# Performance work log

Measured on AMD Instinct MI355X. Metric: run time of the kernel, lower is better.

## Reference

```python
import jax, jax.numpy as jnp
import numpy as np

B, T, X, H, Z, Y, G = 4096, 32, 256, 256, 128, 2, 128


def setup_inputs() -> dict:
    key = jax.random.key(0)
    ks = jax.random.split(key, 16)
    rn = lambda k, s, sc=0.05: jax.random.normal(k, s, dtype=jnp.float32) * sc
    n_days = jnp.concatenate([jnp.array([T], dtype=jnp.int32),
                              jax.random.randint(ks[2], (B - 1,), 1, T + 1).astype(jnp.int32)])
    return {
        "x": rn(ks[0], (B, T, X), 1.0),
        "y_true": jax.nn.softmax(jax.random.normal(ks[1], (B, T, Y), dtype=jnp.float32), axis=-1),
        "n_days": n_days,
        "z0": rn(ks[3], (B, Z), 1.0),
        "eps": rn(ks[4], (T, B, Z), 1.0),
        "W_ih": rn(ks[5], (3 * H, X)), "W_hh": rn(ks[6], (3 * H, H)),
        "b_ih": jnp.zeros((3 * H,), jnp.float32), "b_hh": jnp.zeros((3 * H,), jnp.float32),
        "Wph": rn(ks[7], (Z, X + H + Z)), "bph": jnp.zeros((Z,), jnp.float32),
        "Woh": rn(ks[8], (Z, X + H + Y + Z)), "boh": jnp.zeros((Z,), jnp.float32),
        "Wpm": rn(ks[9], (Z, Z)), "bpm": jnp.zeros((Z,), jnp.float32),
        "Wps": rn(ks[10], (Z, Z)), "bps": jnp.zeros((Z,), jnp.float32),
        "Wqm": rn(ks[11], (Z, Z)), "bqm": jnp.zeros((Z,), jnp.float32),
        "Wqs": rn(ks[12], (Z, Z)), "bqs": jnp.zeros((Z,), jnp.float32),
        "Wg": rn(ks[13], (G, H + Z)), "bg": jnp.zeros((G,), jnp.float32),
        "Wy": rn(ks[14], (Y, G)), "by": jnp.zeros((Y,), jnp.float32),
    }


def _forward(x, y_true, z0, eps, W_ih, W_hh, b_ih, b_hh, Wph, bph, Woh, boh,
             Wpm, bpm, Wps, bps, Wqm, bqm, Wqs, bqs, Wg, bg, Wy, by, n_days):
    xt = jnp.transpose(x, (1, 0, 2))       # [T, B, X]
    yt = jnp.transpose(y_true, (1, 0, 2))  # [T, B, Y]

    # --- GRU over time (torch nn.GRU gate math) ---
    def gru_step(h, xi):
        gi = xi @ W_ih.T + b_ih
        gh = h @ W_hh.T + b_hh
        ir, iz, inn = jnp.split(gi, 3, axis=-1)
        hr, hz, hn = jnp.split(gh, 3, axis=-1)
        r = jax.nn.sigmoid(ir + hr)
        u = jax.nn.sigmoid(iz + hz)
        n = jnp.tanh(inn + r * hn)
        h_new = (1.0 - u) * n + u * h
        return h_new, h_new

    h0 = jnp.zeros((x.shape[0], H), x.dtype)
    _, hs = jax.lax.scan(gru_step, h0, xt)  # [T, B, H]
    # pack/pad semantics: padded timesteps produce zero outputs
    valid = jnp.arange(T)[:, None] < n_days[None, :]  # [T, B]
    hs = jnp.where(valid[:, :, None], hs, 0.0)

    # --- sequential VAE latent scan: z_t depends on z_{t-1} ---
    def vmd_step(z, inputs):
        xi, hi, yi, ei = inputs
        hzp = jnp.tanh(jnp.concatenate([xi, hi, z], -1) @ Wph.T + bph)
        mp = hzp @ Wpm.T + bpm
        sp = jnp.sqrt(jnp.exp(hzp @ Wps.T + bps))
        hzq = jnp.tanh(jnp.concatenate([xi, hi, yi, z], -1) @ Woh.T + boh)
        mq = hzq @ Wqm.T + bqm
        sq = jnp.sqrt(jnp.exp(hzq @ Wqs.T + bqs))
        z_post = mq + sq * ei
        # kl_normal_normal(post || prior)
        kl = jnp.log(sp / sq) + (sq * sq + (mq - mp) ** 2) / (2.0 * sp * sp) - 0.5
        return z_post, (z_post, kl)

    _, (z_posts, kls_e) = jax.lax.scan(vmd_step, z0, (xt, hs, yt, eps))
    kls = jnp.sum(kls_e, axis=-1).T  # [B, T]

    hz = jnp.concatenate([jnp.transpose(hs, (1, 0, 2)),
                          jnp.transpose(z_posts, (1, 0, 2))], -1)  # [B, T, H+Z]
    g = jnp.tanh(hz @ Wg.T + bg)                     # [B, T, G]
    y_pred = jax.nn.softmax(g @ Wy.T + by, axis=-1)  # [B, T, Y]

    idx = n_days - 1
    b = jnp.arange(x.shape[0])
    g_T = g[b, idx]       # [B, G]
    y_T = y_pred[b, idx]  # [B, Y]
    return jnp.concatenate([g_T, y_T, kls], axis=-1)  # [B, G+Y+T]


def reference(x, y_true, n_days, z0, eps, W_ih, W_hh, b_ih, b_hh, Wph, bph,
              Woh, boh, Wpm, bpm, Wps, bps, Wqm, bqm, Wqs, bqs, Wg, bg, Wy, by):
    return _forward(x, y_true, z0, eps, W_ih, W_hh, b_ih, b_hh, Wph, bph, Woh,
                    boh, Wpm, bpm, Wps, bps, Wqm, bqm, Wqs, bqs, Wg, bg, Wy, by,
                    n_days)
```

## Files before the change

### kernel.cpp

```cpp
#include <hip/hip_runtime.h>

typedef unsigned short u16;
typedef short bf16x8 __attribute__((ext_vector_type(8)));
typedef float f32x4 __attribute__((ext_vector_type(4)));

__device__ __forceinline__ float bf2f(u16 v){
  union { unsigned u; float f; } x; x.u = ((unsigned)v) << 16; return x.f;
}
__device__ __forceinline__ u16 f2bf(float f){
  union { float f; unsigned u; } x; x.f = f;
  unsigned u = x.u;
  u += 0x7fffu + ((u >> 16) & 1u);
  return (u16)(u >> 16);
}
__device__ __forceinline__ unsigned pk_bf16(float lo, float hi){
  unsigned r;
  asm volatile("v_cvt_pk_bf16_f32 %0, %1, %2" : "=v"(r) : "v"(lo), "v"(hi));
  return r;
}
__device__ __forceinline__ float sigm(float x){ return 1.f/(1.f+__expf(-x)); }
__device__ __forceinline__ float tanh_s(float x){ return 1.f - 2.f/(__expf(2.f*x)+1.f); }
__device__ __forceinline__ f32x4 mfma16(bf16x8 a, bf16x8 b, f32x4 c){
  return __builtin_amdgcn_mfma_f32_16x16x32_bf16(a, b, c, 0, 0, 0);
}
__device__ __forceinline__ void gl2lds16(const void* g, void* l){
  __builtin_amdgcn_global_load_lds(
      (const __attribute__((address_space(1))) unsigned int*)g,
      (__attribute__((address_space(3))) unsigned int*)l, 16, 0, 0);
}

__global__ void prep_w(const float* __restrict__ W_ih, const float* __restrict__ W_hh,
                       const float* __restrict__ Wph, const float* __restrict__ Woh,
                       const float* __restrict__ Wpm, const float* __restrict__ Wps,
                       const float* __restrict__ Wqm, const float* __restrict__ Wqs,
                       const float* __restrict__ Wg,  const float* __restrict__ bph,
                       const float* __restrict__ boh,
                       u16* __restrict__ wsb, float* __restrict__ Woy, float* __restrict__ bpq)
{
  int idx = blockIdx.x*256 + threadIdx.x;
  if (idx < 196608){ wsb[idx] = f2bf(W_ih[idx]); return; }
  if (idx < 393216){ wsb[idx] = f2bf(W_hh[idx-196608]); return; }
  if (idx < 524288){ int j = idx-393216; int row = j>>9, col = j&511;
    float v = (row<128) ? Wph[row*640+col] : Woh[(row-128)*642+col];
    wsb[idx] = f2bf(v); return; }
  if (idx < 540672){ int j = idx-524288; int row=j>>7, col=j&127; wsb[idx]=f2bf(Wph[row*640+512+col]); return; }
  if (idx < 557056){ int j = idx-540672; int row=j>>7, col=j&127; wsb[idx]=f2bf(Woh[row*642+514+col]); return; }
  if (idx < 573440){ wsb[idx]=f2bf(Wpm[idx-557056]); return; }
  if (idx < 589824){ wsb[idx]=f2bf(Wps[idx-573440]); return; }
  if (idx < 606208){ wsb[idx]=f2bf(Wqm[idx-589824]); return; }
  if (idx < 622592){ wsb[idx]=f2bf(Wqs[idx-606208]); return; }
  if (idx < 671744){ wsb[idx]=f2bf(Wg[idx-622592]); return; }
  if (idx < 672000){ int j = idx-671744; int row=j>>1; Woy[j] = Woh[row*642+512+(j&1)]; return; }
  if (idx < 672256){ int j = idx-672000; bpq[j] = (j<128) ? bph[j] : boh[j-128]; return; }
}

__global__ void prep_b(const float* __restrict__ b_ih, const float* __restrict__ b_hh,
                       float* __restrict__ bsum)
{
  int j = threadIdx.x;
  if (j < 768) bsum[j] = b_ih[j] + (j < 512 ? b_hh[j] : 0.f);
}

__global__ void prep_x(const float* __restrict__ x, u16* __restrict__ xbf){
  int i = blockIdx.x*256 + threadIdx.x;
  if (i >= 4194304) return;
  const float4* src = (const float4*)(x + (size_t)i*8);
  float4 a = src[0], b = src[1];
  uint4 o;
  o.x = pk_bf16(a.x, a.y);
  o.y = pk_bf16(a.z, a.w);
  o.z = pk_bf16(b.x, b.y);
  o.w = pk_bf16(b.z, b.w);
  ((uint4*)xbf)[i] = o;
}

__global__ void sort_days(const int* __restrict__ n_days, int* __restrict__ perm,
                          int* __restrict__ nd_s, int* __restrict__ cnt)
{
  __shared__ int hist[34];
  __shared__ int base[34];
  __shared__ int cursor[34];
  int tid = threadIdx.x;
  if (tid < 34) hist[tid] = 0;
  __syncthreads();
  for (int i = tid; i < 4096; i += 1024) atomicAdd(&hist[n_days[i]], 1);
  __syncthreads();
  if (tid == 0){
    int acc = 0;
    for (int v = 32; v >= 1; --v){ base[v] = acc; acc += hist[v]; }
    base[0] = acc;
  }
  __syncthreads();
  if (tid < 33) cursor[tid] = base[tid];
  if (tid < 32) cnt[tid] = base[tid];
  __syncthreads();
  for (int i = tid; i < 4096; i += 1024){
    int v = n_days[i];
    int pos = atomicAdd(&cursor[v], 1);
    perm[pos] = i;
    nd_s[pos] = v;
  }
}

__global__ __launch_bounds__(512, 4) void gemm_gi(
  const u16* __restrict__ A, const u16* __restrict__ W,
  const float* __restrict__ bias, const int* __restrict__ perm,
  const int* __restrict__ cnt, u16* __restrict__ C)
{
  const int t  = blockIdx.x >> 5;
  const int rt = blockIdx.x & 31;
  if (rt*128 >= cnt[t]) return;
  const int n0 = blockIdx.y*256;
  const int tid = threadIdx.x;
  const int w = tid>>6, lane = tid&63, c = lane&15, g = lane>>4;
  const int wm = w>>2, wn = w&3;
  __shared__ __align__(16) char smem[49152];
  u16* abuf = (u16*)smem;
  u16* wbuf = (u16*)(smem + 16384);
  u16* clds = (u16*)smem;

  size_t asrc[2];
  #pragma unroll
  for (int i=0;i<2;++i){
    int p = (w*2+i)*64 + lane;
    int k8 = p>>7, row = p&127;
    asrc[i] = ((size_t)perm[rt*128 + row]*32 + t)*256 + k8*8;
  }
  size_t wsrc[4];
  #pragma unroll
  for (int i=0;i<4;++i){
    int p = (w*4+i)*64 + lane;
    int k8 = p>>8, row = p&255;
    wsrc[i] = (size_t)(n0+row)*256 + k8*8;
  }
  f32x4 acc[4][4];
  #pragma unroll
  for (int i=0;i<4;++i)
    #pragma unroll
    for (int j=0;j<4;++j) acc[i][j] = (f32x4){0.f,0.f,0.f,0.f};
  for (int kc=0; kc<4; ++kc){
    __syncthreads();
    #pragma unroll
    for (int i=0;i<2;++i) gl2lds16(A + asrc[i] + kc*64, &abuf[(w*2+i)*512]);
    #pragma unroll
    for (int i=0;i<4;++i) gl2lds16(W + wsrc[i] + kc*64, &wbuf[(w*4+i)*512]);
    __syncthreads();
    #pragma unroll
    for (int ks=0;ks<2;++ks){
      int k8 = ks*4 + g;
      bf16x8 a[4];
      #pragma unroll
      for (int mt=0;mt<4;++mt) a[mt] = *(const bf16x8*)&abuf[(k8*128 + wm*64 + mt*16 + c)*8];
      #pragma unroll
      for (int nt=0;nt<4;++nt){
        bf16x8 b = *(const bf16x8*)&wbuf[(k8*256 + wn*64 + nt*16 + c)*8];
        #pragma unroll
        for (int mt=0;mt<4;++mt)
          acc[mt][nt] = mfma16(a[mt], b, acc[mt][nt]);
      }
    }
  }
  __syncthreads();
  const size_t crow = (size_t)t*4096 + rt*128;
  #pragma unroll
  for (int nh=0; nh<2; ++nh){
    if ((wn>>1) == nh){
      #pragma unroll
      for (int nt=0;nt<4;++nt){
        int n = n0 + wn*64 + nt*16 + c;
        float bn = bias[n];
        int lc = (wn&1)*64 + nt*16 + c;
        #pragma unroll
        for (int mt=0;mt<4;++mt){
          int lr = wm*64 + mt*16 + g*4;
          #pragma unroll
          for (int r=0;r<4;++r)
            clds[(lr+r)*136 + lc] = f2bf(acc[mt][nt][r] + bn);
        }
      }
    }
    __syncthreads();
    #pragma unroll
    for (int p=0;p<4;++p){
      int idx = p*512 + tid;
      int row = idx>>4, ch = idx&15;
      *(uint4*)(C + (crow+row)*768 + n0 + nh*128 + ch*8)
        = *(const uint4*)&clds[row*136 + ch*8];
    }
    __syncthreads();
  }
}

__global__ __launch_bounds__(512, 4) void gemm_hpq(
  const u16* __restrict__ A1, const u16* __restrict__ A2,
  const u16* __restrict__ W, const float* __restrict__ bias,
  const float* __restrict__ yt, const float* __restrict__ Woy,
  u16* __restrict__ C)
{
  const int m0 = blockIdx.x*128;
  const int tid = threadIdx.x;
  const int w = tid>>6, lane = tid&63, c = lane&15, g = lane>>4;
  const int wm = w>>2, wn = w&3;
  __shared__ __align__(16) char smem[49152];
  u16* abuf = (u16*)smem;
  u16* wbuf = (u16*)(smem + 16384);
  u16* clds = (u16*)smem;

  size_t asrc[2];
  #pragma unroll
  for (int i=0;i<2;++i){
    int p = (w*2+i)*64 + lane;
    int k8 = p>>7, row = p&127;
    asrc[i] = (size_t)(m0+row)*256 + k8*8;
  }
  size_t wsrc[4];
  #pragma unroll
  for (int i=0;i<4;++i){
    int p = (w*4+i)*64 + lane;
    int k8 = p>>8, row = p&255;
    wsrc[i] = (size_t)row*512 + k8*8;
  }
  f32x4 acc[4][4];
  #pragma unroll
  for (int i=0;i<4;++i)
    #pragma unroll
    for (int j=0;j<4;++j) acc[i][j] = (f32x4){0.f,0.f,0.f,0.f};
  for (int kc=0; kc<8; ++kc){
    __syncthreads();
    const u16* Ab = (kc < 4) ? A1 : A2;
    int ko = (kc & 3)*64;
    #pragma unroll
    for (int i=0;i<2;++i) gl2lds16(Ab + asrc[i] + ko, &abuf[(w*2+i)*512]);
    #pragma unroll
    for (int i=0;i<4;++i) gl2lds16(W + wsrc[i] + kc*64, &wbuf[(w*4+i)*512]);
    __syncthreads();
    #pragma unroll
    for (int ks=0;ks<2;++ks){
      int k8 = ks*4 + g;
      bf16x8 a[4];
      #pragma unroll
      for (int mt=0;mt<4;++mt) a[mt] = *(const bf16x8*)&abuf[(k8*128 + wm*64 + mt*16 + c)*8];
      #pragma unroll
      for (int nt=0;nt<4;++nt){
        bf16x8 b = *(const bf16x8*)&wbuf[(k8*256 + wn*64 + nt*16 + c)*8];
        #pragma unroll
        for (int mt=0;mt<4;++mt)
          acc[mt][nt] = mfma16(a[mt], b, acc[mt][nt]);
      }
    }
  }
  __syncthreads();
  #pragma unroll
  for (int nh=0; nh<2; ++nh){
    if ((wn>>1) == nh){
      #pragma unroll
      for (int nt=0;nt<4;++nt){
        int n = wn*64 + nt*16 + c;
        float bn = bias[n];
        float wy0 = 0.f, wy1 = 0.f;
        bool yfl = (n >= 128);
        if (yfl){ wy0 = Woy[(n-128)*2]; wy1 = Woy[(n-128)*2+1]; }
        int lc = (wn&1)*64 + nt*16 + c;
        #pragma unroll
        for (int mt=0;mt<4;++mt){
          int lr = wm*64 + mt*16 + g*4;
          #pragma unroll
          for (int r=0;r<4;++r){
            size_t m = (size_t)m0 + lr + r;
            float v = acc[mt][nt][r] + bn;
            if (yfl) v += yt[2*m]*wy0 + yt[2*m+1]*wy1;
            clds[(lr+r)*136 + lc] = f2bf(v);
          }
        }
      }
    }
    __syncthreads();
    #pragma unroll
    for (int p=0;p<4;++p){
      int idx = p*512 + tid;
      int row = idx>>4, ch = idx&15;
      *(uint4*)(C + (size_t)(m0+row)*256 + nh*128 + ch*8)
        = *(const uint4*)&clds[row*136 + ch*8];
    }
    __syncthreads();
  }
}

__global__ __launch_bounds__(1024, 4) void gru_seq(
  const u16* __restrict__ GI, const u16* __restrict__ Whh,
  const float* __restrict__ bhh, const int* __restrict__ perm,
  const int* __restrict__ nd_s, u16* __restrict__ hs)
{
  const int b0 = blockIdx.x*16;
  const int tid = threadIdx.x;
  const int w = tid>>6, lane = tid&63, c = lane&15, g = lane>>4;
  const int j0 = w*16 + g*4;
  __shared__ __align__(16) u16 hbuf[2][4096];
  __shared__ __align__(16) u16 gibuf[3][12288];
  __shared__ float bhnl[256];

  bf16x8 wa[3][8];
  #pragma unroll
  for (int gate=0; gate<3; ++gate)
    #pragma unroll
    for (int ks=0; ks<8; ++ks)
      wa[gate][ks] = *(const bf16x8*)&Whh[(size_t)(gate*256 + w*16 + c)*256 + ks*32 + g*8];

  if (tid < 256) bhnl[tid] = bhh[512 + tid];
  const int ndc   = nd_s[b0 + c];
  const int bound = nd_s[b0];
  const int ob    = perm[b0 + c];

  int so0, so1;
  { int pe = w*512 + lane*8; int row = pe/768, off = pe - row*768;
    so0 = (b0+row)*768 + (off ^ ((row&7)<<3)); }
  { int pe = (16+w)*512 + lane*8; int row = pe/768, off = pe - row*768;
    so1 = (b0+row)*768 + (off ^ ((row&7)<<3)); }
  const int rd0 = c*1536 + ((j0*2) ^ ((c&7)<<4));
  const int hroff = (g*16 + c)*16;
  const int hwoff = ((w*2 + (g>>1))*16 + c)*16 + (g&1)*8;
  u16* hsp = hs + (size_t)ob*8192 + j0;

  float hprev[4] = {0.f,0.f,0.f,0.f};
  if (tid < 512) ((uint4*)hbuf[0])[tid] = make_uint4(0,0,0,0);

  const size_t PL = 3145728;
  int p1 = (bound > 1) ? 1 : 0;
  gl2lds16(GI + so0, (char*)gibuf[0] + w*1024);
  if (w < 8) gl2lds16(GI + so1, (char*)gibuf[0] + (16+w)*1024);
  gl2lds16(GI + (size_t)p1*PL + so0, (char*)gibuf[1] + w*1024);
  if (w < 8) gl2lds16(GI + (size_t)p1*PL + so1, (char*)gibuf[1] + (16+w)*1024);
  asm volatile("s_waitcnt vmcnt(0)" ::: "memory");
  __syncthreads();

  const u16* hr = hbuf[0];
  u16*       hw = hbuf[1];
  int cur = 0;
  #pragma unroll 1
  for (int t=0; t<bound; ++t){
    {
      int pf = (t+2 < bound) ? t+2 : bound-1;
      int nxt3 = cur >= 1 ? cur-1 : 2;
      gl2lds16(GI + (size_t)pf*PL + so0, (char*)gibuf[nxt3] + w*1024);
      if (w < 8) gl2lds16(GI + (size_t)pf*PL + so1, (char*)gibuf[nxt3] + (16+w)*1024);
    }
    const char* gib = (const char*)gibuf[cur];
    ushort4 gr_ = *(const ushort4*)(gib + rd0);
    ushort4 gu_ = *(const ushort4*)(gib + rd0 + 512);
    ushort4 gn_ = *(const ushort4*)(gib + rd0 + 1024);
    if (w < 8) asm volatile("s_waitcnt vmcnt(3)" ::: "memory");
    else       asm volatile("s_waitcnt vmcnt(2)" ::: "memory");
    __builtin_amdgcn_sched_barrier(0);
    f32x4 aR = (f32x4){0.f,0.f,0.f,0.f};
    f32x4 aU = (f32x4){0.f,0.f,0.f,0.f};
    float4 bhn4 = *(const float4*)&bhnl[j0];
    f32x4 aN = (f32x4){bhn4.x, bhn4.y, bhn4.z, bhn4.w};
    __builtin_amdgcn_s_setprio(1);
    #pragma unroll
    for (int ks=0; ks<8; ++ks){
      bf16x8 hf = *(const bf16x8*)((const char*)hr + hroff + ks*1024);
      aR = mfma16(wa[0][ks], hf, aR);
      aU = mfma16(wa[1][ks], hf, aU);
      aN = mfma16(wa[2][ks], hf, aN);
    }
    __builtin_amdgcn_s_setprio(0);
    {
      float h4[4];
      #pragma unroll
      for (int r=0; r<4; ++r){
        u16 grv = r==0?gr_.x : r==1?gr_.y : r==2?gr_.z : gr_.w;
        u16 guv = r==0?gu_.x : r==1?gu_.y : r==2?gu_.z : gu_.w;
        u16 gnv = r==0?gn_.x : r==1?gn_.y : r==2?gn_.z : gn_.w;
        float rr = sigm(bf2f(grv) + aR[r]);
        float uu = sigm(bf2f(guv) + aU[r]);
        float nn = tanh_s(bf2f(gnv) + rr*aN[r]);
        float h = nn + uu*(hprev[r]-nn);
        hprev[r] = h;
        h4[r] = h;
      }
      uint2 hpk;
      hpk.x = pk_bf16(h4[0], h4[1]);
      hpk.y = pk_bf16(h4[2], h4[3]);
      *(uint2*)((char*)hw + hwoff) = hpk;
      uint2 hst = (t < ndc) ? hpk : make_uint2(0u,0u);
      *(uint2*)(hsp + t*256) = hst;
    }
    asm volatile("s_waitcnt lgkmcnt(0)" ::: "memory");
    __builtin_amdgcn_sched_barrier(0);
    __builtin_amdgcn_s_barrier();
    __builtin_amdgcn_sched_barrier(0);
    { const u16* tmp = hr; hr = hw; hw = (u16*)tmp; }
    cur = cur==2 ? 0 : cur+1;
  }
  for (int t=bound; t<32; ++t)
    *(uint2*)(hsp + t*256) = make_uint2(0u,0u);
}

__global__ __launch_bounds__(512) void vae_seq(
  const u16* __restrict__ HPQ, const float* __restrict__ z0,
  const float* __restrict__ eps, const int* __restrict__ n_days,
  const u16* __restrict__ Wm,
  const float* __restrict__ bpm, const float* __restrict__ bps,
  const float* __restrict__ bqm, const float* __restrict__ bqs,
  u16* __restrict__ zidx, float* __restrict__ out)
{
  const int b0 = blockIdx.x*16;
  const int tid = threadIdx.x, w = tid>>6, lane = tid&63, c = lane&15, g = lane>>4;
  const int j0 = w*16 + g*4;
  __shared__ __align__(16) u16 zbuf[16*16*8];
  __shared__ __align__(16) u16 hzpb[16*16*8];
  __shared__ __align__(16) u16 hzqb[16*16*8];
  __shared__ __align__(16) char hpql[3][8192];
  __shared__ __align__(16) char epsl[3][8192];
  __shared__ float klb[32][16][8];

  bf16x8 wf[6][4];
  #pragma unroll
  for (int mat=0;mat<6;++mat)
    #pragma unroll
    for (int ks=0;ks<4;++ks)
      wf[mat][ks] = *(const bf16x8*)&Wm[mat*16384 + (w*16+c)*128 + ks*32 + g*8];

  const float4 bpm4 = *(const float4*)(bpm + j0);
  const float4 bps4 = *(const float4*)(bps + j0);
  const float4 bqm4 = *(const float4*)(bqm + j0);
  const float4 bqs4 = *(const float4*)(bqs + j0);
  const int ndc = n_days[b0 + c];

  int soH, soE;
  { int p = (w*64 + lane)*16; int row = p/512, off = p%512;
    int so = off ^ ((row&7)<<4);
    soH = (b0+row)*32*256 + (so>>1);
    soE = (b0+row)*128 + (so>>2); }
  const int rdH = c*512 + ((j0*2) ^ ((c&7)<<4));
  const int rdE = c*512 + ((j0*4) ^ ((c&7)<<4));
  const int hroff = (g*16 + c)*16;
  const int hwoff = ((w*2 + (g>>1))*16 + c)*16 + (g&1)*8;

  if (tid < 256){
    int k8 = tid>>4, row = tid&15;
    const float* zp = z0 + (size_t)(b0+row)*128 + k8*8;
    uint4 o;
    o.x = pk_bf16(zp[0], zp[1]);
    o.y = pk_bf16(zp[2], zp[3]);
    o.z = pk_bf16(zp[4], zp[5]);
    o.w = pk_bf16(zp[6], zp[7]);
    ((uint4*)zbuf)[tid] = o;
  }
  gl2lds16(HPQ + soH,          hpql[0] + w*1024);
  gl2lds16(eps + soE,          epsl[0] + w*1024);
  gl2lds16(HPQ + soH + 256,    hpql[1] + w*1024);
  gl2lds16(eps + soE + 524288, epsl[1] + w*1024);
  asm volatile("s_waitcnt vmcnt(0)" ::: "memory");
  __syncthreads();

  uint2 zsel = make_uint2(0u,0u);
  int cur = 0;
  #pragma unroll 1
  for (int t=0; t<32; ++t){
    if (t < 30){
      int nxt3 = cur >= 1 ? cur-1 : 2;
      gl2lds16(HPQ + soH + (t+2)*256,            hpql[nxt3] + w*1024);
      gl2lds16(eps + soE + (size_t)(t+2)*524288, epsl[nxt3] + w*1024);
    }
    if (t < 30)      { asm volatile("s_waitcnt vmcnt(2)" ::: "memory"); }
    else if (t == 30){ asm volatile("s_waitcnt vmcnt(0)" ::: "memory"); }
    __builtin_amdgcn_sched_barrier(0);
    f32x4 accP = (f32x4){0,0,0,0}, accQ = (f32x4){0,0,0,0};
    #pragma unroll
    for (int ks=0;ks<4;++ks){
      bf16x8 zf = *(const bf16x8*)((const char*)zbuf + hroff + ks*1024);
      accP = mfma16(wf[0][ks], zf, accP);
      accQ = mfma16(wf[1][ks], zf, accQ);
    }
    {
      const char* hb_ = hpql[cur];
      ushort4 hp4 = *(const ushort4*)(hb_ + rdH);
      ushort4 hq4 = *(const ushort4*)(hb_ + rdH + 256);
      float p4[4], q4[4];
      #pragma unroll
      for (int r=0;r<4;++r){
        u16 pv = r==0?hp4.x : r==1?hp4.y : r==2?hp4.z : hp4.w;
        u16 qv = r==0?hq4.x : r==1?hq4.y : r==2?hq4.z : hq4.w;
        p4[r] = tanh_s(bf2f(pv) + accP[r]);
        q4[r] = tanh_s(bf2f(qv) + accQ[r]);
      }
      uint2 ppk, qpk;
      ppk.x = pk_bf16(p4[0], p4[1]);  ppk.y = pk_bf16(p4[2], p4[3]);
      qpk.x = pk_bf16(q4[0], q4[1]);  qpk.y = pk_bf16(q4[2], q4[3]);
      *(uint2*)((char*)hzpb + hwoff) = ppk;
      *(uint2*)((char*)hzqb + hwoff) = qpk;
    }
    asm volatile("s_waitcnt lgkmcnt(0)" ::: "memory");
    __builtin_amdgcn_sched_barrier(0);
    __builtin_amdgcn_s_barrier();
    __builtin_amdgcn_sched_barrier(0);
    {
      f32x4 aMP=(f32x4){0,0,0,0}, aAP=(f32x4){0,0,0,0};
      f32x4 aMQ=(f32x4){0,0,0,0}, aAQ=(f32x4){0,0,0,0};
      #pragma unroll
      for (int ks=0;ks<4;++ks){
        bf16x8 pf = *(const bf16x8*)((const char*)hzpb + hroff + ks*1024);
        bf16x8 qf = *(const bf16x8*)((const char*)hzqb + hroff + ks*1024);
        aMP = mfma16(wf[2][ks], pf, aMP);
        aAP = mfma16(wf[3][ks], pf, aAP);
        aMQ = mfma16(wf[4][ks], qf, aMQ);
        aAQ = mfma16(wf[5][ks], qf, aAQ);
      }
      float4 e4 = *(const float4*)(epsl[cur] + rdE);
      float kls = 0.f;
      float z4[4];
      #pragma unroll
      for (int r=0;r<4;++r){
        float mp = aMP[r]+(r==0?bpm4.x:r==1?bpm4.y:r==2?bpm4.z:bpm4.w);
        float ap = aAP[r]+(r==0?bps4.x:r==1?bps4.y:r==2?bps4.z:bps4.w);
        float mq = aMQ[r]+(r==0?bqm4.x:r==1?bqm4.y:r==2?bqm4.z:bqm4.w);
        float aq = aAQ[r]+(r==0?bqs4.x:r==1?bqs4.y:r==2?bqs4.z:bqs4.w);
        float ev = r==0?e4.x : r==1?e4.y : r==2?e4.z : e4.w;
        float z = mq + __expf(0.5f*aq)*ev;
        float d = mq - mp;
        kls += 0.5f*(ap-aq) + 0.5f*(__expf(aq)+d*d)*__expf(-ap) - 0.5f;
        z4[r] = z;
      }
      uint2 zpk;
      zpk.x = pk_bf16(z4[0], z4[1]);
      zpk.y = pk_bf16(z4[2], z4[3]);
      *(uint2*)((char*)zbuf + hwoff) = zpk;
      if (t == ndc-1) zsel = zpk;
      kls += __shfl_xor(kls, 16);
      kls += __shfl_xor(kls, 32);
      if (lane < 16) klb[t][c][w] = kls;
    }
    asm volatile("s_waitcnt lgkmcnt(0)" ::: "memory");
    __builtin_amdgcn_sched_barrier(0);
    __builtin_amdgcn_s_barrier();
    __builtin_amdgcn_sched_barrier(0);
    cur = cur==2 ? 0 : cur+1;
  }
  *(uint2*)(zidx + (size_t)(b0+c)*128 + j0) = zsel;
  {
    int t2 = tid>>4, c2 = tid&15;
    float s = 0.f;
    #pragma unroll
    for (int ww=0;ww<8;++ww) s += klb[t2][c2][ww];
    out[(size_t)(b0+c2)*162 + 130 + t2] = s;
  }
}

__global__ __launch_bounds__(128) void head_k(
  const u16* __restrict__ hs, const u16* __restrict__ zidx,
  const int* __restrict__ n_days, const u16* __restrict__ Wgb,
  const float* __restrict__ bg, const float* __restrict__ Wy,
  const float* __restrict__ by, float* __restrict__ out)
{
  const int b = blockIdx.x;
  const int tid = threadIdx.x;
  const int lane = tid & 63, wv = tid >> 6;
  __shared__ float hz[384];
  __shared__ float red[2][2];
  const int idx = n_days[b]-1;
  const u16* hrow = hs + ((size_t)b*32 + idx)*256;
  for (int k=tid; k<256; k+=128) hz[k] = bf2f(hrow[k]);
  hz[256+tid] = bf2f(zidx[(size_t)b*128 + tid]);
  __syncthreads();
  const u16* wrow = Wgb + (size_t)tid*384;
  float s = 0.f;
  #pragma unroll 4
  for (int k8=0;k8<48;++k8){
    bf16x8 wvv = *(const bf16x8*)&wrow[k8*8];
    #pragma unroll
    for (int e=0;e<8;++e) s += bf2f((u16)wvv[e]) * hz[k8*8+e];
  }
  float gv = tanh_s(s + bg[tid]);
  out[(size_t)b*162 + tid] = gv;
  float a0 = gv*Wy[tid], a1 = gv*Wy[128+tid];
  #pragma unroll
  for (int off=1; off<64; off<<=1){
    a0 += __shfl_xor(a0, off);
    a1 += __shfl_xor(a1, off);
  }
  if (lane == 0){ red[0][wv] = a0; red[1][wv] = a1; }
  __syncthreads();
  if (tid == 0){
    float l0 = by[0] + red[0][0] + red[0][1];
    float l1 = by[1] + red[1][0] + red[1][1];
    float mx = fmaxf(l0,l1);
    float e0 = __expf(l0-mx), e1 = __expf(l1-mx);
    float si = e0+e1;
    out[(size_t)b*162 + 128] = e0/si;
    out[(size_t)b*162 + 129] = e1/si;
  }
}

extern "C" void kernel_launch(void* const* d_in, const int* in_sizes, int n_in,
                              void* d_out, int out_size, void* d_ws, size_t ws_size,
                              hipStream_t stream)
{
  const float* x      = (const float*)d_in[0];
  const float* y_true = (const float*)d_in[1];
  const int*   n_days = (const int*)d_in[2];
  const float* z0     = (const float*)d_in[3];
  const float* eps    = (const float*)d_in[4];
  const float* W_ih   = (const float*)d_in[5];
  const float* W_hh   = (const float*)d_in[6];
  const float* b_ih   = (const float*)d_in[7];
  const float* b_hh   = (const float*)d_in[8];
  const float* Wph    = (const float*)d_in[9];
  const float* bph    = (const float*)d_in[10];
  const float* Woh    = (const float*)d_in[11];
  const float* boh    = (const float*)d_in[12];
  const float* Wpm    = (const float*)d_in[13];
  const float* bpm    = (const float*)d_in[14];
  const float* Wps    = (const float*)d_in[15];
  const float* bps    = (const float*)d_in[16];
  const float* Wqm    = (const float*)d_in[17];
  const float* bqm    = (const float*)d_in[18];
  const float* Wqs    = (const float*)d_in[19];
  const float* bqs    = (const float*)d_in[20];
  const float* Wg     = (const float*)d_in[21];
  const float* bg     = (const float*)d_in[22];
  const float* Wy     = (const float*)d_in[23];
  const float* by     = (const float*)d_in[24];
  (void)in_sizes; (void)n_in; (void)out_size; (void)ws_size;

  u16*   wsb = (u16*)d_ws;
  float* wsf = (float*)d_ws;
  int*   wsi = (int*)d_ws;
  u16* Wih_b = wsb + 0;
  u16* Whh_b = wsb + 196608;
  u16* Wc_b  = wsb + 393216;
  u16* Wz_b  = wsb + 524288;
  u16* Wg_b  = wsb + 622592;
  float* Woy  = wsf + 335872;
  float* bpq  = wsf + 336128;
  float* bsum = wsf + 336384;
  int* perm   = wsi + 337152;
  int* nd_s   = wsi + 341248;
  int* cnt    = wsi + 345344;
  u16* xbf   = wsb + 690752;
  u16* GI    = wsb + 34245184;
  u16* hsB   = wsb + 134908480;
  u16* HPQ   = wsb + 168462912;
  u16* zidx  = wsb + 202017344;

  hipLaunchKernelGGL(prep_w, dim3(2626), dim3(256), 0, stream,
                     W_ih, W_hh, Wph, Woh, Wpm, Wps, Wqm, Wqs, Wg, bph, boh,
                     wsb, Woy, bpq);
  hipLaunchKernelGGL(prep_b, dim3(1), dim3(768), 0, stream, b_ih, b_hh, bsum);
  hipLaunchKernelGGL(prep_x, dim3(16384), dim3(256), 0, stream, x, xbf);
  hipLaunchKernelGGL(sort_days, dim3(1), dim3(1024), 0, stream,
                     n_days, perm, nd_s, cnt);
  hipLaunchKernelGGL(gemm_gi, dim3(1024,3), dim3(512), 0, stream,
                     xbf, Wih_b, bsum, perm, cnt, GI);
  hipLaunchKernelGGL(gru_seq, dim3(256), dim3(1024), 0, stream,
                     GI, Whh_b, b_hh, perm, nd_s, hsB);
  hipLaunchKernelGGL(gemm_hpq, dim3(1024), dim3(512), 0, stream,
                     xbf, hsB, Wc_b, bpq, y_true, Woy, HPQ);
  hipLaunchKernelGGL(vae_seq, dim3(256), dim3(512), 0, stream,
                     HPQ, z0, eps, n_days, Wz_b, bpm, bps, bqm, bqs, zidx, (float*)d_out);
  hipLaunchKernelGGL(head_k, dim3(4096), dim3(128), 0, stream,
                     hsB, zidx, n_days, Wg_b, bg, Wy, by, (float*)d_out);
}
```

Measured before the change: 510.3 us.

## Replace LDS-staged prefetch with register double-buffered direct global loads in recurrences

The GRU and VAE recurrent kernels used to stream per-step gate inputs and eps/HPQ slices through triple-buffered LDS via global_load_lds, with explicit vmcnt waits. They now load each thread's slice straight into registers two steps ahead, ping-ponging between two register sets across a manually unrolled loop. The LDS staging buffers and the bias LDS copy are removed, and the GRU launch-bounds occupancy hint is dropped. This aims to cut LDS traffic and waitcnt stalls, at the cost of more VGPRs and less coalesced 8-byte global loads whose latency must be hidden by one step of compute.

```diff
diff --git a/kernel.cpp b/kernel.cpp
--- a/kernel.cpp
+++ b/kernel.cpp
@@ -15,9 +15,11 @@
 }
 __device__ __forceinline__ unsigned pk_bf16(float lo, float hi){
   unsigned r;
-  asm volatile("v_cvt_pk_bf16_f32 %0, %1, %2" : "=v"(r) : "v"(lo), "v"(hi));
+  asm("v_cvt_pk_bf16_f32 %0, %1, %2" : "=v"(r) : "v"(lo), "v"(hi));
   return r;
 }
+__device__ __forceinline__ u16 el4(ushort4 v, int r){ return r==0?v.x:r==1?v.y:r==2?v.z:v.w; }
+__device__ __forceinline__ float elf4(float4 v, int r){ return r==0?v.x:r==1?v.y:r==2?v.z:v.w; }
 __device__ __forceinline__ float sigm(float x){ return 1.f/(1.f+__expf(-x)); }
 __device__ __forceinline__ float tanh_s(float x){ return 1.f - 2.f/(__expf(2.f*x)+1.f); }
 __device__ __forceinline__ f32x4 mfma16(bf16x8 a, bf16x8 b, f32x4 c){
@@ -286,7 +288,7 @@
   }
 }
 
-__global__ __launch_bounds__(1024, 4) void gru_seq(
+__global__ __launch_bounds__(1024) void gru_seq(
   const u16* __restrict__ GI, const u16* __restrict__ Whh,
   const float* __restrict__ bhh, const int* __restrict__ perm,
   const int* __restrict__ nd_s, u16* __restrict__ hs)
@@ -296,8 +298,6 @@
   const int w = tid>>6, lane = tid&63, c = lane&15, g = lane>>4;
   const int j0 = w*16 + g*4;
   __shared__ __align__(16) u16 hbuf[2][4096];
-  __shared__ __align__(16) u16 gibuf[3][12288];
-  __shared__ float bhnl[256];
 
   bf16x8 wa[3][8];
   #pragma unroll
@@ -306,54 +306,38 @@
     for (int ks=0; ks<8; ++ks)
       wa[gate][ks] = *(const bf16x8*)&Whh[(size_t)(gate*256 + w*16 + c)*256 + ks*32 + g*8];
 
-  if (tid < 256) bhnl[tid] = bhh[512 + tid];
+  const float4 bhn4 = *(const float4*)(bhh + 512 + j0);
   const int ndc   = nd_s[b0 + c];
   const int bound = nd_s[b0];
   const int ob    = perm[b0 + c];
 
-  int so0, so1;
-  { int pe = w*512 + lane*8; int row = pe/768, off = pe - row*768;
-    so0 = (b0+row)*768 + (off ^ ((row&7)<<3)); }
-  { int pe = (16+w)*512 + lane*8; int row = pe/768, off = pe - row*768;
-    so1 = (b0+row)*768 + (off ^ ((row&7)<<3)); }
-  const int rd0 = c*1536 + ((j0*2) ^ ((c&7)<<4));
   const int hroff = (g*16 + c)*16;
   const int hwoff = ((w*2 + (g>>1))*16 + c)*16 + (g&1)*8;
   u16* hsp = hs + (size_t)ob*8192 + j0;
+  const size_t PL = 3145728;
+  const u16* gib = GI + (size_t)(b0+c)*768 + j0;
 
   float hprev[4] = {0.f,0.f,0.f,0.f};
   if (tid < 512) ((uint4*)hbuf[0])[tid] = make_uint4(0,0,0,0);
 
-  const size_t PL = 3145728;
-  int p1 = (bound > 1) ? 1 : 0;
-  gl2lds16(GI + so0, (char*)gibuf[0] + w*1024);
-  if (w < 8) gl2lds16(GI + so1, (char*)gibuf[0] + (16+w)*1024);
-  gl2lds16(GI + (size_t)p1*PL + so0, (char*)gibuf[1] + w*1024);
-  if (w < 8) gl2lds16(GI + (size_t)p1*PL + so1, (char*)gibuf[1] + (16+w)*1024);
-  asm volatile("s_waitcnt vmcnt(0)" ::: "memory");
+  ushort4 gA[3], gB[3];
+  gA[0] = *(const ushort4*)(gib);
+  gA[1] = *(const ushort4*)(gib + 256);
+  gA[2] = *(const ushort4*)(gib + 512);
+  {
+    const u16* g1 = gib + ((bound > 1) ? PL : 0);
+    gB[0] = *(const ushort4*)(g1);
+    gB[1] = *(const ushort4*)(g1 + 256);
+    gB[2] = *(const ushort4*)(g1 + 512);
+  }
   __syncthreads();
 
   const u16* hr = hbuf[0];
   u16*       hw = hbuf[1];
-  int cur = 0;
-  #pragma unroll 1
-  for (int t=0; t<bound; ++t){
-    {
-      int pf = (t+2 < bound) ? t+2 : bound-1;
-      int nxt3 = cur >= 1 ? cur-1 : 2;
-      gl2lds16(GI + (size_t)pf*PL + so0, (char*)gibuf[nxt3] + w*1024);
-      if (w < 8) gl2lds16(GI + (size_t)pf*PL + so1, (char*)gibuf[nxt3] + (16+w)*1024);
-    }
-    const char* gib = (const char*)gibuf[cur];
-    ushort4 gr_ = *(const ushort4*)(gib + rd0);
-    ushort4 gu_ = *(const ushort4*)(gib + rd0 + 512);
-    ushort4 gn_ = *(const ushort4*)(gib + rd0 + 1024);
-    if (w < 8) asm volatile("s_waitcnt vmcnt(3)" ::: "memory");
-    else       asm volatile("s_waitcnt vmcnt(2)" ::: "memory");
-    __builtin_amdgcn_sched_barrier(0);
+
+  auto step = [&](ushort4 (&gs)[3], int t){
     f32x4 aR = (f32x4){0.f,0.f,0.f,0.f};
     f32x4 aU = (f32x4){0.f,0.f,0.f,0.f};
-    float4 bhn4 = *(const float4*)&bhnl[j0];
     f32x4 aN = (f32x4){bhn4.x, bhn4.y, bhn4.z, bhn4.w};
     __builtin_amdgcn_s_setprio(1);
     #pragma unroll
@@ -364,36 +348,44 @@
       aN = mfma16(wa[2][ks], hf, aN);
     }
     __builtin_amdgcn_s_setprio(0);
+    float h4[4];
+    #pragma unroll
+    for (int r=0; r<4; ++r){
+      float rr = sigm(bf2f(el4(gs[0],r)) + aR[r]);
+      float uu = sigm(bf2f(el4(gs[1],r)) + aU[r]);
+      float nn = tanh_s(bf2f(el4(gs[2],r)) + rr*aN[r]);
+      float h = nn + uu*(hprev[r]-nn);
+      hprev[r] = h;
+      h4[r] = h;
+    }
+    uint2 hpk;
+    hpk.x = pk_bf16(h4[0], h4[1]);
+    hpk.y = pk_bf16(h4[2], h4[3]);
+    *(uint2*)((char*)hw + hwoff) = hpk;
+    *(uint2*)(hsp + t*256) = (t < ndc) ? hpk : make_uint2(0u,0u);
     {
-      float h4[4];
-      #pragma unroll
-      for (int r=0; r<4; ++r){
-        u16 grv = r==0?gr_.x : r==1?gr_.y : r==2?gr_.z : gr_.w;
-        u16 guv = r==0?gu_.x : r==1?gu_.y : r==2?gu_.z : gu_.w;
-        u16 gnv = r==0?gn_.x : r==1?gn_.y : r==2?gn_.z : gn_.w;
-        float rr = sigm(bf2f(grv) + aR[r]);
-        float uu = sigm(bf2f(guv) + aU[r]);
-        float nn = tanh_s(bf2f(gnv) + rr*aN[r]);
-        float h = nn + uu*(hprev[r]-nn);
-        hprev[r] = h;
-        h4[r] = h;
-      }
-      uint2 hpk;
-      hpk.x = pk_bf16(h4[0], h4[1]);
-      hpk.y = pk_bf16(h4[2], h4[3]);
-      *(uint2*)((char*)hw + hwoff) = hpk;
-      uint2 hst = (t < ndc) ? hpk : make_uint2(0u,0u);
-      *(uint2*)(hsp + t*256) = hst;
+      int pf = (t+2 < bound) ? t+2 : bound-1;
+      const u16* gp = gib + (size_t)pf*PL;
+      gs[0] = *(const ushort4*)(gp);
+      gs[1] = *(const ushort4*)(gp + 256);
+      gs[2] = *(const ushort4*)(gp + 512);
     }
     asm volatile("s_waitcnt lgkmcnt(0)" ::: "memory");
     __builtin_amdgcn_sched_barrier(0);
     __builtin_amdgcn_s_barrier();
     __builtin_amdgcn_sched_barrier(0);
-    { const u16* tmp = hr; hr = hw; hw = (u16*)tmp; }
-    cur = cur==2 ? 0 : cur+1;
-  }
-  for (int t=bound; t<32; ++t)
-    *(uint2*)(hsp + t*256) = make_uint2(0u,0u);
+    const u16* tmp = hr; hr = hw; hw = (u16*)tmp;
+  };
+
+  int t = 0;
+  for (;;){
+    step(gA, t);
+    if (++t >= bound) break;
+    step(gB, t);
+    if (++t >= bound) break;
+  }
+  for (int t2 = bound; t2 < 32; ++t2)
+    *(uint2*)(hsp + t2*256) = make_uint2(0u,0u);
 }
 
 __global__ __launch_bounds__(512) void vae_seq(
@@ -410,8 +402,6 @@
   __shared__ __align__(16) u16 zbuf[16*16*8];
   __shared__ __align__(16) u16 hzpb[16*16*8];
   __shared__ __align__(16) u16 hzqb[16*16*8];
-  __shared__ __align__(16) char hpql[3][8192];
-  __shared__ __align__(16) char epsl[3][8192];
   __shared__ float klb[32][16][8];
 
   bf16x8 wf[6][4];
@@ -427,15 +417,10 @@
   const float4 bqs4 = *(const float4*)(bqs + j0);
   const int ndc = n_days[b0 + c];
 
-  int soH, soE;
-  { int p = (w*64 + lane)*16; int row = p/512, off = p%512;
-    int so = off ^ ((row&7)<<4);
-    soH = (b0+row)*32*256 + (so>>1);
-    soE = (b0+row)*128 + (so>>2); }
-  const int rdH = c*512 + ((j0*2) ^ ((c&7)<<4));
-  const int rdE = c*512 + ((j0*4) ^ ((c&7)<<4));
   const int hroff = (g*16 + c)*16;
   const int hwoff = ((w*2 + (g>>1))*16 + c)*16 + (g&1)*8;
+  const u16*  hbp = HPQ + ((size_t)(b0+c)*32)*256 + j0;
+  const float* ebp = eps + (size_t)(b0+c)*128 + j0;
 
   if (tid < 256){
     int k8 = tid>>4, row = tid&15;
@@ -447,25 +432,18 @@
     o.w = pk_bf16(zp[6], zp[7]);
     ((uint4*)zbuf)[tid] = o;
   }
-  gl2lds16(HPQ + soH,          hpql[0] + w*1024);
-  gl2lds16(eps + soE,          epsl[0] + w*1024);
-  gl2lds16(HPQ + soH + 256,    hpql[1] + w*1024);
-  gl2lds16(eps + soE + 524288, epsl[1] + w*1024);
-  asm volatile("s_waitcnt vmcnt(0)" ::: "memory");
-  __syncthreads();
+  __syncthreads();
+
+  ushort4 pA = *(const ushort4*)(hbp);
+  ushort4 qA = *(const ushort4*)(hbp + 128);
+  float4  eA = *(const float4*)(ebp);
+  ushort4 pB = *(const ushort4*)(hbp + 256);
+  ushort4 qB = *(const ushort4*)(hbp + 384);
+  float4  eB = *(const float4*)(ebp + 524288);
 
   uint2 zsel = make_uint2(0u,0u);
-  int cur = 0;
-  #pragma unroll 1
-  for (int t=0; t<32; ++t){
-    if (t < 30){
-      int nxt3 = cur >= 1 ? cur-1 : 2;
-      gl2lds16(HPQ + soH + (t+2)*256,            hpql[nxt3] + w*1024);
-      gl2lds16(eps + soE + (size_t)(t+2)*524288, epsl[nxt3] + w*1024);
-    }
-    if (t < 30)      { asm volatile("s_waitcnt vmcnt(2)" ::: "memory"); }
-    else if (t == 30){ asm volatile("s_waitcnt vmcnt(0)" ::: "memory"); }
-    __builtin_amdgcn_sched_barrier(0);
+
+  auto step = [&](ushort4& hp4, ushort4& hq4, float4& e4, int t){
     f32x4 accP = (f32x4){0,0,0,0}, accQ = (f32x4){0,0,0,0};
     #pragma unroll
     for (int ks=0;ks<4;++ks){
@@ -473,70 +451,71 @@
       accP = mfma16(wf[0][ks], zf, accP);
       accQ = mfma16(wf[1][ks], zf, accQ);
     }
-    {
-      const char* hb_ = hpql[cur];
-      ushort4 hp4 = *(const ushort4*)(hb_ + rdH);
-      ushort4 hq4 = *(const ushort4*)(hb_ + rdH + 256);
-      float p4[4], q4[4];
-      #pragma unroll
-      for (int r=0;r<4;++r){
-        u16 pv = r==0?hp4.x : r==1?hp4.y : r==2?hp4.z : hp4.w;
-        u16 qv = r==0?hq4.x : r==1?hq4.y : r==2?hq4.z : hq4.w;
-        p4[r] = tanh_s(bf2f(pv) + accP[r]);
-        q4[r] = tanh_s(bf2f(qv) + accQ[r]);
-      }
-      uint2 ppk, qpk;
-      ppk.x = pk_bf16(p4[0], p4[1]);  ppk.y = pk_bf16(p4[2], p4[3]);
-      qpk.x = pk_bf16(q4[0], q4[1]);  qpk.y = pk_bf16(q4[2], q4[3]);
-      *(uint2*)((char*)hzpb + hwoff) = ppk;
-      *(uint2*)((char*)hzqb + hwoff) = qpk;
-    }
+    float p4[4], q4[4];
+    #pragma unroll
+    for (int r=0;r<4;++r){
+      p4[r] = tanh_s(bf2f(el4(hp4,r)) + accP[r]);
+      q4[r] = tanh_s(bf2f(el4(hq4,r)) + accQ[r]);
+    }
+    uint2 ppk, qpk;
+    ppk.x = pk_bf16(p4[0], p4[1]);  ppk.y = pk_bf16(p4[2], p4[3]);
+    qpk.x = pk_bf16(q4[0], q4[1]);  qpk.y = pk_bf16(q4[2], q4[3]);
+    *(uint2*)((char*)hzpb + hwoff) = ppk;
+    *(uint2*)((char*)hzqb + hwoff) = qpk;
     asm volatile("s_waitcnt lgkmcnt(0)" ::: "memory");
     __builtin_amdgcn_sched_barrier(0);
     __builtin_amdgcn_s_barrier();
     __builtin_amdgcn_sched_barrier(0);
-    {
-      f32x4 aMP=(f32x4){0,0,0,0}, aAP=(f32x4){0,0,0,0};
-      f32x4 aMQ=(f32x4){0,0,0,0}, aAQ=(f32x4){0,0,0,0};
-      #pragma unroll
-      for (int ks=0;ks<4;++ks){
-        bf16x8 pf = *(const bf16x8*)((const char*)hzpb + hroff + ks*1024);
-        bf16x8 qf = *(const bf16x8*)((const char*)hzqb + hroff + ks*1024);
-        aMP = mfma16(wf[2][ks], pf, aMP);
-        aAP = mfma16(wf[3][ks], pf, aAP);
-        aMQ = mfma16(wf[4][ks], qf, aMQ);
-        aAQ = mfma16(wf[5][ks], qf, aAQ);
-      }
-      float4 e4 = *(const float4*)(epsl[cur] + rdE);
-      float kls = 0.f;
-      float z4[4];
-      #pragma unroll
-      for (int r=0;r<4;++r){
-        float mp = aMP[r]+(r==0?bpm4.x:r==1?bpm4.y:r==2?bpm4.z:bpm4.w);
-        float ap = aAP[r]+(r==0?bps4.x:r==1?bps4.y:r==2?bps4.z:bps4.w);
-        float mq = aMQ[r]+(r==0?bqm4.x:r==1?bqm4.y:r==2?bqm4.z:bqm4.w);
-        float aq = aAQ[r]+(r==0?bqs4.x:r==1?bqs4.y:r==2?bqs4.z:bqs4.w);
-        float ev = r==0?e4.x : r==1?e4.y : r==2?e4.z : e4.w;
-        float z = mq + __expf(0.5f*aq)*ev;
-        float d = mq - mp;
-        kls += 0.5f*(ap-aq) + 0.5f*(__expf(aq)+d*d)*__expf(-ap) - 0.5f;
-        z4[r] = z;
-      }
-      uint2 zpk;
-      zpk.x = pk_bf16(z4[0], z4[1]);
-      zpk.y = pk_bf16(z4[2], z4[3]);
-      *(uint2*)((char*)zbuf + hwoff) = zpk;
-      if (t == ndc-1) zsel = zpk;
-      kls += __shfl_xor(kls, 16);
-      kls += __shfl_xor(kls, 32);
-      if (lane < 16) klb[t][c][w] = kls;
+    f32x4 aMP=(f32x4){0,0,0,0}, aAP=(f32x4){0,0,0,0};
+    f32x4 aMQ=(f32x4){0,0,0,0}, aAQ=(f32x4){0,0,0,0};
+    #pragma unroll
+    for (int ks=0;ks<4;++ks){
+      bf16x8 pf = *(const bf16x8*)((const char*)hzpb + hroff + ks*1024);
+      bf16x8 qf = *(const bf16x8*)((const char*)hzqb + hroff + ks*1024);
+      aMP = mfma16(wf[2][ks], pf, aMP);
+      aAP = mfma16(wf[3][ks], pf, aAP);
+      aMQ = mfma16(wf[4][ks], qf, aMQ);
+      aAQ = mfma16(wf[5][ks], qf, aAQ);
+    }
+    float kls = 0.f;
+    float z4[4];
+    #pragma unroll
+    for (int r=0;r<4;++r){
+      float mp = aMP[r]+elf4(bpm4,r);
+      float ap = aAP[r]+elf4(bps4,r);
+      float mq = aMQ[r]+elf4(bqm4,r);
+      float aq = aAQ[r]+elf4(bqs4,r);
+      float ev = elf4(e4,r);
+      float z = mq + __expf(0.5f*aq)*ev;
+      float d = mq - mp;
+      kls += 0.5f*(ap-aq) + 0.5f*(__expf(aq)+d*d)*__expf(-ap) - 0.5f;
+      z4[r] = z;
+    }
+    uint2 zpk;
+    zpk.x = pk_bf16(z4[0], z4[1]);
+    zpk.y = pk_bf16(z4[2], z4[3]);
+    *(uint2*)((char*)zbuf + hwoff) = zpk;
+    if (t == ndc-1) zsel = zpk;
+    kls += __shfl_xor(kls, 16);
+    kls += __shfl_xor(kls, 32);
+    if (lane < 16) klb[t][c][w] = kls;
+    if (t < 30){
+      hp4 = *(const ushort4*)(hbp + (t+2)*256);
+      hq4 = *(const ushort4*)(hbp + (t+2)*256 + 128);
+      e4  = *(const float4*)(ebp + (size_t)(t+2)*524288);
     }
     asm volatile("s_waitcnt lgkmcnt(0)" ::: "memory");
     __builtin_amdgcn_sched_barrier(0);
     __builtin_amdgcn_s_barrier();
     __builtin_amdgcn_sched_barrier(0);
-    cur = cur==2 ? 0 : cur+1;
-  }
+  };
+
+  #pragma unroll 1
+  for (int t=0; t<32; t+=2){
+    step(pA, qA, eA, t);
+    step(pB, qB, eB, t+1);
+  }
+
   *(uint2*)(zidx + (size_t)(b0+c)*128 + j0) = zsel;
   {
     int t2 = tid>>4, c2 = tid&15;
```

Result: slower. 537.3 us (+5.3%).
